# Optimization experiments

Hardware: AMD Instinct MI355X
Metric: run time of the kernel (lower is better)

Reference implementation:

```python
import jax, jax.numpy as jnp
import numpy as np

E = 6          # num_experts
TOP_K = 2
FUT = 60       # future_len
DIM = 128

def _gelu(x):
    return jax.nn.gelu(x, approximate=False)  # torch nn.GELU default is exact erf


def setup_inputs() -> dict:
    key = jax.random.key(0)
    ks = jax.random.split(key, 20)
    B, M, D = 8192, 6, DIM
    s = 0.02
    inp = {
        "mode_features": jax.random.normal(ks[0], (B, M, D), jnp.float32),
        # router MLP: D->256->128->E  (dropout is identity in eval mode)
        "rW1": jax.random.normal(ks[1], (D, 256)) * s, "rb1": jnp.zeros((256,)),
        "rW2": jax.random.normal(ks[2], (256, 128)) * s, "rb2": jnp.zeros((128,)),
        "rW3": jax.random.normal(ks[3], (128, E)) * s, "rb3": jnp.zeros((E,)),
        # stacked expert trajectory heads: D->256->256->2*FUT
        "tW1": jax.random.normal(ks[4], (E, D, 256)) * s, "tb1": jnp.zeros((E, 256)),
        "tW2": jax.random.normal(ks[5], (E, 256, 256)) * s, "tb2": jnp.zeros((E, 256)),
        "tW3": jax.random.normal(ks[6], (E, 256, 2 * FUT)) * s, "tb3": jnp.zeros((E, 2 * FUT)),
        # stacked expert score heads: D->128->64->1
        "sW1": jax.random.normal(ks[7], (E, D, 128)) * s, "sb1": jnp.zeros((E, 128)),
        "sW2": jax.random.normal(ks[8], (E, 128, 64)) * s, "sb2": jnp.zeros((E, 64)),
        "sW3": jax.random.normal(ks[9], (E, 64, 1)) * s, "sb3": jnp.zeros((E, 1)),
    }
    return {k: v.astype(jnp.float32) for k, v in inp.items()}


def reference(mode_features, rW1, rb1, rW2, rb2, rW3, rb3,
              tW1, tb1, tW2, tb2, tW3, tb3,
              sW1, sb1, sW2, sb2, sW3, sb3):
    B, M, D = mode_features.shape
    x = mode_features.reshape(B * M, D)  # [N, D]

    # ---- router (dropout = identity at inference) ----
    h = _gelu(x @ rW1 + rb1)
    h = _gelu(h @ rW2 + rb2)
    logits = h @ rW3 + rb3                      # [N, E]
    router_probs = jax.nn.softmax(logits, axis=-1)

    top_v, top_i = jax.lax.top_k(logits, TOP_K)  # [N, K]
    top_w = jax.nn.softmax(top_v, axis=-1)       # renormalized top-k weights

    # ---- all experts, dense over E (then gather top-k) ----
    th = _gelu(jnp.einsum('nd,edh->neh', x, tW1) + tb1)   # [N, E, 256]
    th = _gelu(jnp.einsum('neh,ehg->neg', th, tW2) + tb2) # [N, E, 256]
    traj_all = jnp.einsum('neh,eho->neo', th, tW3) + tb3  # [N, E, 2*FUT]

    sh = _gelu(jnp.einsum('nd,edh->neh', x, sW1) + sb1)   # [N, E, 128]
    sh = _gelu(jnp.einsum('neh,ehg->neg', sh, sW2) + sb2) # [N, E, 64]
    score_all = (jnp.einsum('neh,eho->neo', sh, sW3) + sb3)[..., 0]  # [N, E]

    traj_sel = jnp.take_along_axis(traj_all, top_i[:, :, None], axis=1)  # [N, K, 2*FUT]
    score_sel = jnp.take_along_axis(score_all, top_i, axis=1)            # [N, K]

    trajectories = (top_w[:, :, None] * traj_sel).sum(axis=1).reshape(B, M, FUT, 2)
    scores = (top_w * score_sel).sum(axis=1).reshape(B, M)

    # ---- load-balance aux loss ----
    avg_probs = router_probs.mean(axis=0)  # [E]
    entropy = -(avg_probs * jnp.log(avg_probs + 1e-8)).sum()
    lb_loss = -entropy * 0.01
    l2_loss = jnp.mean((avg_probs - 1.0 / E) ** 2)
    aux_loss = lb_loss + 0.01 * l2_loss

    return trajectories, scores, aux_loss, router_probs.reshape(B, M, E)
```

## Files before the change

### kernel.cpp

```cpp
#include <hip/hip_runtime.h>

#define N_TOK 49152
#define PER_E 155648
#define NSTAGE 19
#define RSTAGES 24
#define MAXTILES 774

#define TRAJ_OFF 0
#define SCORE_OFF 5898240
#define AUX_OFF  5947392
#define PROB_OFF 5947393

typedef __attribute__((ext_vector_type(8))) short short8v;
typedef __attribute__((ext_vector_type(4))) float f32x4;
typedef __attribute__((ext_vector_type(4))) unsigned short u16x4;

typedef __attribute__((address_space(3))) unsigned char lds_byte;
typedef __attribute__((address_space(1))) const unsigned char gl_byte;

__device__ __forceinline__ unsigned short f2bf(float f) {
  unsigned int u = __float_as_uint(f);
  u = (u + 0x7FFFu + ((u >> 16) & 1u)) >> 16;
  return (unsigned short)u;
}
__device__ __forceinline__ float bf2f(unsigned short h) {
  return __uint_as_float(((unsigned int)h) << 16);
}
__device__ __forceinline__ unsigned int pkbf(float a, float b) {
  unsigned int r;
  asm("v_cvt_pk_bf16_f32 %0, %1, %2" : "=v"(r) : "v"(a), "v"(b));
  return r;
}
__device__ __forceinline__ float geluf(float v) {
  float x = v * 0.70710678118654752f;
  float ax = fabsf(x);
  float t = __builtin_amdgcn_rcpf(fmaf(0.3275911f, ax, 1.0f));
  float p = t * fmaf(t, fmaf(t, fmaf(t, fmaf(t, 1.061405429f, -1.453152027f),
                                     1.421413741f), -0.284496736f), 0.254829592f);
  float er = 1.0f - p * __expf(-ax * ax);
  er = copysignf(er, x);
  return 0.5f * v * (1.0f + er);
}
__device__ __forceinline__ float geluf_fast(float v) {
  float x = v * 0.70710678f;
  float ax = fabsf(x);
  float t = __builtin_amdgcn_rcpf(fmaf(0.47047f, ax, 1.0f));
  float poly = t * fmaf(t, fmaf(t, 0.7478556f, -0.0958798f), 0.3480242f);
  float er = fmaf(-poly, __expf(-ax * ax), 1.0f);
  er = copysignf(er, x);
  return 0.5f * v * (1.0f + er);
}

__global__ __launch_bounds__(256) void prep_weights(
    const float* __restrict__ tW1, const float* __restrict__ tW2, const float* __restrict__ tW3,
    const float* __restrict__ sW1, const float* __restrict__ sW2,
    unsigned short* __restrict__ blob)
{
  int id = blockIdx.x * 256 + threadIdx.x;
  if (id >= 6 * PER_E) return;
  int e = id / PER_E;
  int r = id - e * PER_E;
  int p = r >> 13;
  int q = r & 8191;
  int f = q >> 9;
  int l = (q >> 3) & 63;
  int j = q & 7;
  int hi = l >> 4, rl = l & 15;
  const float* src; int N, tile, ks; bool perm;
  if (p < 2)       { src = sW1 + e * 16384; N = 128; tile = 4 * p + (f >> 2);        ks = f & 3; perm = false; }
  else if (p == 2) { src = sW2 + e * 8192;  N = 64;  tile = f >> 2;                  ks = f & 3; perm = true;  }
  else if (p < 7)  { src = tW1 + e * 32768; N = 256; tile = 4 * (p - 3) + (f >> 2);  ks = f & 3; perm = false; }
  else if (p < 11) { src = tW2 + e * 65536; N = 256; tile = 2 * (p - 7) + (f >> 3);  ks = f & 7; perm = true;  }
  else if (p < 13) { src = tW3 + e * 30720; N = 120; tile = f >> 1;  ks = 2 * (p - 11) + (f & 1); perm = true; }
  else if (p < 17) { src = tW2 + e * 65536; N = 256; tile = 8 + 2 * (p - 13) + (f >> 3); ks = f & 7; perm = true; }
  else             { src = tW3 + e * 30720; N = 120; tile = f >> 1;  ks = 4 + 2 * (p - 17) + (f & 1); perm = true; }
  int k = ks * 32 + (perm ? (16 * (j >> 2) + 4 * hi + (j & 3)) : (8 * hi + j));
  int unit = tile * 16 + rl;
  blob[id] = f2bf(unit < N ? src[k * N + unit] : 0.0f);
}

__global__ __launch_bounds__(256) void prep_router(
    const float* __restrict__ rW1, const float* __restrict__ rW2,
    unsigned short* __restrict__ rblob)
{
  int id = blockIdx.x * 256 + threadIdx.x;
  if (id >= RSTAGES * 8192) return;
  int p = id >> 13;
  int q = id & 8191;
  int f = q >> 9;
  int l = (q >> 3) & 63;
  int j = q & 7;
  int hi = l >> 4, rl = l & 15;
  const float* src; int N, tile, ks, part; bool perm;
  if (p < 12) { int c = p / 3; part = p % 3; src = rW1; N = 256; tile = 4 * c + (f >> 2); ks = f & 3; perm = false; }
  else        { int c = (p - 12) / 3; part = (p - 12) % 3; src = rW2; N = 128; tile = 2 * c + (f >> 3); ks = f & 7; perm = true; }
  int k = ks * 32 + (perm ? (16 * (j >> 2) + 4 * hi + (j & 3)) : (8 * hi + j));
  int unit = tile * 16 + rl;
  float v = (unit < N) ? src[k * N + unit] : 0.0f;
  unsigned short b0 = f2bf(v);
  float r1 = v - bf2f(b0);
  unsigned short b1 = f2bf(r1);
  float r2 = r1 - bf2f(b1);
  unsigned short b2 = f2bf(r2);
  rblob[id] = (part == 0) ? b0 : ((part == 1) ? b1 : b2);
}

__device__ __forceinline__ f32x4 MM16(short8v a, short8v b, f32x4 c) {
  return __builtin_amdgcn_mfma_f32_16x16x32_bf16(a, b, c, 0, 0, 0);
}
__device__ __forceinline__ void cvt16(f32x4 aE, f32x4 aO, const float* bp, int hi, short8v& fr) {
  float g[8];
  #pragma unroll
  for (int j = 0; j < 8; ++j) {
    float v = (j < 4) ? aE[j & 3] : aO[j & 3];
    int unit = 16 * (j >> 2) + 4 * hi + (j & 3);
    g[j] = geluf_fast(v + bp[unit]);
  }
  unsigned int* pr = (unsigned int*)&fr;
  pr[0] = pkbf(g[0], g[1]); pr[1] = pkbf(g[2], g[3]);
  pr[2] = pkbf(g[4], g[5]); pr[3] = pkbf(g[6], g[7]);
}
__device__ __forceinline__ void cvt16s(f32x4 aE, f32x4 aO, const float* bp, int hi,
                                       short8v& f0, short8v& f1) {
  #pragma unroll
  for (int j = 0; j < 8; ++j) {
    float v = (j < 4) ? aE[j & 3] : aO[j & 3];
    int unit = 16 * (j >> 2) + 4 * hi + (j & 3);
    float g = geluf(v + bp[unit]);
    unsigned short b0 = f2bf(g);
    f0[j] = (short)b0;
    f1[j] = (short)f2bf(g - bf2f(b0));
  }
}

#define RFRAG(s, f) (*(const short8v*)(&wlds[((s) % 3) * 8192 + (f) * 512 + lane * 8]))

#define RSTAGE(s) do { \
    const unsigned short* gsrc_ = rblob + (s) * 8192 + w * 1024 + lane * 8; \
    unsigned short* ldst_ = &wlds[((s) % 3) * 8192 + w * 1024]; \
    _Pragma("unroll") \
    for (int i_ = 0; i_ < 2; ++i_) \
      __builtin_amdgcn_global_load_lds((gl_byte*)(gsrc_ + i_ * 512), (lds_byte*)(ldst_ + i_ * 512), 16, 0, 0); \
  } while (0)

#define RPIPE(s, nw) do { \
    asm volatile("s_waitcnt vmcnt(" #nw ")" ::: "memory"); \
    __builtin_amdgcn_sched_barrier(0); \
    __builtin_amdgcn_s_barrier(); \
    __builtin_amdgcn_sched_barrier(0); \
    if ((s) + 2 < RSTAGES) RSTAGE((s) + 2); \
  } while (0)

__global__ __launch_bounds__(512, 4) void router_mfma(
    const float* __restrict__ x, const unsigned short* __restrict__ rblob,
    const float* __restrict__ rb1, const float* __restrict__ rb2,
    const float* __restrict__ rW3, const float* __restrict__ rb3,
    float* __restrict__ probs_out,
    int* __restrict__ pairTok, float* __restrict__ pairW, int* __restrict__ pairIdx,
    int* __restrict__ cnt, float* __restrict__ probsum)
{
  __shared__ __align__(16) unsigned short wlds[3 * 8192];
  __shared__ float bLds[1160];
  __shared__ float probsLds[768];
  __shared__ float psum[8];
  __shared__ int lcnt[8], gbase[8];

  int tid = threadIdx.x;
  int lane = tid & 63;
  int w = tid >> 6;
  int col = lane & 15;
  int hi = lane >> 4;
  int tok0 = blockIdx.x * 128;
  int myTok = tok0 + w * 16 + col;

  if (tid < 256) bLds[tid] = rb1[tid];
  else if (tid < 384) bLds[tid] = rb2[tid - 256];
  for (int i = tid; i < 768; i += 512) bLds[384 + i] = rW3[i];
  if (tid < 6) bLds[1152 + tid] = rb3[tid];
  if (tid < 8) { psum[tid] = 0.f; lcnt[tid] = 0; }

  short8v xf0[4], xf1[4], xf2[4];
  {
    const float* px = x + (size_t)myTok * 128 + hi * 8;
    #pragma unroll
    for (int ks = 0; ks < 4; ++ks) {
      f32x4 lo = *(const f32x4*)(px + ks * 32);
      f32x4 hv = *(const f32x4*)(px + ks * 32 + 4);
      #pragma unroll
      for (int j = 0; j < 8; ++j) {
        float v = (j < 4) ? lo[j & 3] : hv[j & 3];
        unsigned short b0 = f2bf(v);
        float r1 = v - bf2f(b0);
        unsigned short b1 = f2bf(r1);
        float r2 = r1 - bf2f(b1);
        xf0[ks][j] = (short)b0;
        xf1[ks][j] = (short)b1;
        xf2[ks][j] = (short)f2bf(r2);
      }
    }
  }
  __syncthreads();

  RSTAGE(0);
  RSTAGE(1);

  short8v h0B[8], h1B[8];
  #pragma unroll
  for (int c = 0; c < 4; ++c) {
    f32x4 acc[4] = {};
    RPIPE(3 * c, 2);
    #pragma unroll
    for (int ks = 0; ks < 4; ++ks)
      #pragma unroll
      for (int u = 0; u < 4; ++u) {
        short8v wf = RFRAG(3 * c, u * 4 + ks);
        acc[u] = MM16(wf, xf0[ks], acc[u]);
        acc[u] = MM16(wf, xf1[ks], acc[u]);
        acc[u] = MM16(wf, xf2[ks], acc[u]);
      }
    RPIPE(3 * c + 1, 2);
    #pragma unroll
    for (int ks = 0; ks < 4; ++ks)
      #pragma unroll
      for (int u = 0; u < 4; ++u) {
        short8v wf = RFRAG(3 * c + 1, u * 4 + ks);
        acc[u] = MM16(wf, xf0[ks], acc[u]);
        acc[u] = MM16(wf, xf1[ks], acc[u]);
      }
    RPIPE(3 * c + 2, 2);
    #pragma unroll
    for (int ks = 0; ks < 4; ++ks)
      #pragma unroll
      for (int u = 0; u < 4; ++u) {
        short8v wf = RFRAG(3 * c + 2, u * 4 + ks);
        acc[u] = MM16(wf, xf0[ks], acc[u]);
      }
    cvt16s(acc[0], acc[1], bLds + 32 * (2 * c),     hi, h0B[2 * c],     h1B[2 * c]);
    cvt16s(acc[2], acc[3], bLds + 32 * (2 * c + 1), hi, h0B[2 * c + 1], h1B[2 * c + 1]);
  }

  f32x4 acc2[8] = {};
  #pragma unroll
  for (int d = 0; d < 4; ++d) {
    RPIPE(12 + 3 * d, 2);
    #pragma unroll
    for (int ks = 0; ks < 8; ++ks)
      #pragma unroll
      for (int u = 0; u < 2; ++u) {
        short8v wf = RFRAG(12 + 3 * d, u * 8 + ks);
        int t = 2 * d + u;
        acc2[t] = MM16(wf, h0B[ks], acc2[t]);
        acc2[t] = MM16(wf, h1B[ks], acc2[t]);
      }
    RPIPE(12 + 3 * d + 1, 2);
    #pragma unroll
    for (int ks = 0; ks < 8; ++ks)
      #pragma unroll
      for (int u = 0; u < 2; ++u) {
        short8v wf = RFRAG(12 + 3 * d + 1, u * 8 + ks);
        int t = 2 * d + u;
        acc2[t] = MM16(wf, h0B[ks], acc2[t]);
        acc2[t] = MM16(wf, h1B[ks], acc2[t]);
      }
    if (d < 3) { RPIPE(12 + 3 * d + 2, 2); }
    else       { RPIPE(23, 0); }
    #pragma unroll
    for (int ks = 0; ks < 8; ++ks)
      #pragma unroll
      for (int u = 0; u < 2; ++u) {
        short8v wf = RFRAG(12 + 3 * d + 2, u * 8 + ks);
        int t = 2 * d + u;
        acc2[t] = MM16(wf, h0B[ks], acc2[t]);
      }
  }

  float pl[6] = {0.f, 0.f, 0.f, 0.f, 0.f, 0.f};
  #pragma unroll
  for (int t = 0; t < 8; ++t)
    #pragma unroll
    for (int r = 0; r < 4; ++r) {
      int unit = t * 16 + 4 * hi + r;
      float h2 = geluf(acc2[t][r] + bLds[256 + unit]);
      #pragma unroll
      for (int e = 0; e < 6; ++e)
        pl[e] = fmaf(h2, bLds[384 + unit * 6 + e], pl[e]);
    }
  #pragma unroll
  for (int e = 0; e < 6; ++e) {
    pl[e] += __shfl_xor(pl[e], 16);
    pl[e] += __shfl_xor(pl[e], 32);
  }

  int i1 = 0, i2 = 0, lp1 = 0, lp2 = 0;
  float ww1 = 0.f, ww2 = 0.f;
  if (hi == 0) {
    float l0[6];
    #pragma unroll
    for (int e = 0; e < 6; ++e) l0[e] = pl[e] + bLds[1152 + e];
    float m = l0[0];
    #pragma unroll
    for (int e = 1; e < 6; ++e) m = fmaxf(m, l0[e]);
    float pe[6]; float ssum = 0.f;
    #pragma unroll
    for (int e = 0; e < 6; ++e) { pe[e] = expf(l0[e] - m); ssum += pe[e]; }
    float inv = 1.f / ssum;
    int lrow = w * 16 + col;
    #pragma unroll
    for (int e = 0; e < 6; ++e) {
      float prb = pe[e] * inv;
      probsLds[lrow * 6 + e] = prb;
      atomicAdd(&psum[e], prb);
    }
    float v1 = l0[0]; i1 = 0; float v2 = -1e30f; i2 = -1;
    #pragma unroll
    for (int e = 1; e < 6; ++e) {
      float v = l0[e];
      if (v > v1) { v2 = v1; i2 = i1; v1 = v; i1 = e; }
      else if (v > v2) { v2 = v; i2 = e; }
    }
    float e2 = expf(v2 - v1);
    float den = 1.f / (1.f + e2);
    ww1 = den; ww2 = e2 * den;
    lp1 = atomicAdd(&lcnt[i1], 1);
    lp2 = atomicAdd(&lcnt[i2], 1);
  }
  __syncthreads();
  if (tid < 6) gbase[tid] = atomicAdd(&cnt[tid], lcnt[tid]);
  __syncthreads();
  if (hi == 0) {
    int g1 = gbase[i1] + lp1, g2 = gbase[i2] + lp2;
    pairTok[i1 * N_TOK + g1] = myTok; pairW[i1 * N_TOK + g1] = ww1;
    pairTok[i2 * N_TOK + g2] = myTok; pairW[i2 * N_TOK + g2] = ww2;
    pairIdx[2 * myTok]     = i1 * N_TOK + g1;
    pairIdx[2 * myTok + 1] = i2 * N_TOK + g2;
  }
  if (tid < 6) atomicAdd(&probsum[tid], psum[tid]);
  for (int i = tid; i < 768; i += 512)
    probs_out[(size_t)tok0 * 6 + i] = probsLds[i];
}

__global__ void aux_kernel(const float* __restrict__ probsum, const int* __restrict__ cnt,
                           int* __restrict__ csum, int* __restrict__ ntiles, int* __restrict__ tiles,
                           float* __restrict__ auxout)
{
  if (threadIdx.x == 0 && blockIdx.x == 0) {
    int s = 0;
    for (int e = 0; e < 6; ++e) { csum[e] = s; s += cnt[e]; }
    int nt = 0;
    for (int e = 0; e < 6; ++e)
      for (int b = 0; b < cnt[e]; b += 256)
        tiles[nt++] = (e << 16) | (b >> 8);
    ntiles[0] = nt;
    float ent = 0.f, l2 = 0.f;
    for (int e = 0; e < 6; ++e) {
      float avg = probsum[e] / (float)N_TOK;
      ent -= avg * logf(avg + 1e-8f);
      float d = avg - (1.0f / 6.0f);
      l2 += d * d;
    }
    l2 *= (1.0f / 6.0f);
    auxout[0] = -ent * 0.01f + 0.01f * l2;
  }
}

#define EFRAG(s, f) (*(const short8v*)(&wlds[((s) & 3) * 8192 + (f) * 512 + lane * 8]))

#define ESTAGE(s) do { \
    const unsigned short* gsrc_ = eblob + (s) * 8192 + w * 512 + lane * 8; \
    unsigned short* ldst_ = &wlds[((s) & 3) * 8192 + w * 512]; \
    __builtin_amdgcn_global_load_lds((gl_byte*)gsrc_, (lds_byte*)ldst_, 16, 0, 0); \
  } while (0)

#define EPIPE(S) do { \
    if (((S) & 1) == 0) { \
      asm volatile("s_waitcnt vmcnt(0)" ::: "memory"); \
      __builtin_amdgcn_sched_barrier(0); \
      __builtin_amdgcn_s_barrier(); \
      __builtin_amdgcn_sched_barrier(0); \
      if ((S) + 2 < NSTAGE) ESTAGE((S) + 2); \
      if ((S) + 3 < NSTAGE) ESTAGE((S) + 3); \
    } \
  } while (0)

template<int OUTMODE>
__global__ __launch_bounds__(1024, 4) void expert_kernel(
    const float* __restrict__ x,
    const unsigned short* __restrict__ blob,
    const float* __restrict__ tb1, const float* __restrict__ tb2, const float* __restrict__ tb3,
    const float* __restrict__ sb1, const float* __restrict__ sb2,
    const float* __restrict__ sW3, const float* __restrict__ sb3,
    const int* __restrict__ pairTok, const float* __restrict__ pairW,
    const int* __restrict__ cnt, const int* __restrict__ csum,
    const int* __restrict__ ntiles, const int* __restrict__ tiles,
    float* __restrict__ traj_out, float* __restrict__ score_out,
    unsigned short* __restrict__ trajP, float* __restrict__ scoreP)
{
  if (blockIdx.x >= (unsigned)ntiles[0]) return;
  int ent = tiles[blockIdx.x];
  int e = ent >> 16;
  int base = (ent & 0xffff) << 8;
  int count = cnt[e];

  __shared__ __align__(16) unsigned short wlds[4 * 8192];
  __shared__ float bLds[896];
  __shared__ int   toksLds[256];
  __shared__ float gwsLds[256];

  int tid = threadIdx.x;
  int lane = tid & 63;
  int w = tid >> 6;
  int col = lane & 15;
  int hi = lane >> 4;
  const unsigned short* eblob = blob + (size_t)e * PER_E;
  int slotbase = csum[e] + base;

  if (tid < 256) {
    int idx = e * N_TOK + base + ((base + tid < count) ? tid : 0);
    toksLds[tid] = pairTok[idx];
    gwsLds[tid] = (base + tid < count) ? pairW[idx] : 0.f;
  }
  if (tid < 128) bLds[tid] = sb1[e * 128 + tid];
  else if (tid < 192) bLds[tid] = sb2[e * 64 + tid - 128];
  else if (tid < 256) bLds[tid] = sW3[e * 64 + tid - 192];
  else if (tid < 512) bLds[tid] = tb1[e * 256 + tid - 256];
  else if (tid < 768) bLds[tid] = tb2[e * 256 + tid - 512];
  else if (tid < 888) bLds[tid] = tb3[e * 120 + tid - 768];
  __syncthreads();

  int row = w * 16 + col;
  int tok = toksLds[row];
  bool valid = (base + row < count);
  float gw = gwsLds[row];

  short8v xf[4];
  {
    const float* px = x + (size_t)tok * 128 + hi * 8;
    #pragma unroll
    for (int ks = 0; ks < 4; ++ks) {
      f32x4 lo = *(const f32x4*)(px + ks * 32);
      f32x4 hv = *(const f32x4*)(px + ks * 32 + 4);
      unsigned int* pt = (unsigned int*)&xf[ks];
      pt[0] = pkbf(lo[0], lo[1]); pt[1] = pkbf(lo[2], lo[3]);
      pt[2] = pkbf(hv[0], hv[1]); pt[3] = pkbf(hv[2], hv[3]);
    }
  }

  ESTAGE(0);
  ESTAGE(1);

  short8v sB[4];
  {
    f32x4 a[4] = {};
    EPIPE(0);
    #pragma unroll
    for (int f = 0; f < 16; ++f)
      a[f >> 2] = MM16(EFRAG(0, f), xf[f & 3], a[f >> 2]);
    cvt16(a[0], a[1], bLds + 0,  hi, sB[0]);  cvt16(a[2], a[3], bLds + 32, hi, sB[1]);
    f32x4 b[4] = {};
    EPIPE(1);
    #pragma unroll
    for (int f = 0; f < 16; ++f)
      b[f >> 2] = MM16(EFRAG(1, f), xf[f & 3], b[f >> 2]);
    cvt16(b[0], b[1], bLds + 64, hi, sB[2]);  cvt16(b[2], b[3], bLds + 96, hi, sB[3]);
  }

  float p0 = 0.f;
  {
    f32x4 q[4] = {};
    EPIPE(2);
    #pragma unroll
    for (int f = 0; f < 16; ++f)
      q[f >> 2] = MM16(EFRAG(2, f), sB[f & 3], q[f >> 2]);
    #pragma unroll
    for (int t = 0; t < 4; ++t)
      #pragma unroll
      for (int r = 0; r < 4; ++r) {
        int unit = t * 16 + 4 * hi + r;
        p0 += geluf_fast(q[t][r] + bLds[128 + unit]) * bLds[192 + unit];
      }
    p0 += __shfl_xor(p0, 16); p0 += __shfl_xor(p0, 32);
  }

  short8v h1B[8];
  #define T1S(t, S) { \
    f32x4 a[4] = {}; \
    EPIPE(S); \
    _Pragma("unroll") \
    for (int f = 0; f < 16; ++f) \
      a[f >> 2] = MM16(EFRAG(S, f), xf[f & 3], a[f >> 2]); \
    cvt16(a[0], a[1], bLds + 256 + (t) * 64,      hi, h1B[2 * (t)]); \
    cvt16(a[2], a[3], bLds + 256 + (t) * 64 + 32, hi, h1B[2 * (t) + 1]); \
  }
  T1S(0, 3) T1S(1, 4) T1S(2, 5) T1S(3, 6)

  short8v h2B[4];
  #define T2S(s, S, BOFF) { \
    f32x4 u[2] = {}; \
    EPIPE(S); \
    _Pragma("unroll") \
    for (int f = 0; f < 16; ++f) \
      u[f >> 3] = MM16(EFRAG(S, f), h1B[f & 7], u[f >> 3]); \
    cvt16(u[0], u[1], bLds + 512 + (BOFF) + 32 * (s), hi, h2B[s]); \
  }

  f32x4 wacc[8] = {};
  #define T3S(s, S) { \
    EPIPE(S); \
    _Pragma("unroll") \
    for (int f = 0; f < 16; ++f) \
      wacc[f >> 1] = MM16(EFRAG(S, f), h2B[2 * (s) + (f & 1)], wacc[f >> 1]); \
  }

  T2S(0, 7, 0) T2S(1, 8, 0) T2S(2, 9, 0) T2S(3, 10, 0)
  T3S(0, 11) T3S(1, 12)
  T2S(0, 13, 128) T2S(1, 14, 128) T2S(2, 15, 128) T2S(3, 16, 128)
  T3S(0, 17) T3S(1, 18)

  if (hi == 0 && valid) {
    float v = gw * (p0 + sb3[e]);
    if (OUTMODE == 0) scoreP[slotbase + row] = v; else atomicAdd(&score_out[tok], v);
  }
  if (valid) {
    if (OUTMODE == 0) {
      unsigned short* dst = trajP + (size_t)(slotbase + row) * 120;
      #pragma unroll
      for (int t = 0; t < 8; ++t)
        #pragma unroll
        for (int r = 0; r < 4; r += 2) {
          int unit = t * 16 + 4 * hi + r;
          if (unit + 1 < 120) {
            float a0 = gw * (wacc[t][r] + bLds[768 + unit]);
            float a1 = gw * (wacc[t][r + 1] + bLds[768 + unit + 1]);
            *(unsigned int*)(dst + unit) = pkbf(a0, a1);
          }
        }
    } else {
      float* dst = traj_out + (size_t)tok * 120;
      #pragma unroll
      for (int t = 0; t < 8; ++t)
        #pragma unroll
        for (int r = 0; r < 4; ++r) {
          int unit = t * 16 + 4 * hi + r;
          if (unit < 120) atomicAdd(&dst[unit], gw * (wacc[t][r] + bLds[768 + unit]));
        }
    }
  }
}

__global__ __launch_bounds__(256) void combine_kernel(
    const int* __restrict__ pairIdx, const int* __restrict__ csum,
    const unsigned short* __restrict__ trajP, const float* __restrict__ scoreP,
    float* __restrict__ traj_out, float* __restrict__ score_out)
{
  int t = blockIdx.x * 256 + threadIdx.x;
  if (t >= N_TOK) return;
  int p0 = pairIdx[2 * t], p1 = pairIdx[2 * t + 1];
  int e0 = p0 / N_TOK, e1 = p1 / N_TOK;
  size_t s0 = (size_t)csum[e0] + (p0 - e0 * N_TOK);
  size_t s1 = (size_t)csum[e1] + (p1 - e1 * N_TOK);
  const unsigned short* r0 = trajP + s0 * 120;
  const unsigned short* r1 = trajP + s1 * 120;
  float* o = traj_out + (size_t)t * 120;
  #pragma unroll 6
  for (int i = 0; i < 30; ++i) {
    u16x4 a = *(const u16x4*)(r0 + i * 4);
    u16x4 b = *(const u16x4*)(r1 + i * 4);
    f32x4 v;
    #pragma unroll
    for (int jj = 0; jj < 4; ++jj) v[jj] = bf2f(a[jj]) + bf2f(b[jj]);
    *(f32x4*)(o + i * 4) = v;
  }
  score_out[t] = scoreP[s0] + scoreP[s1];
}

extern "C" void kernel_launch(void* const* d_in, const int* in_sizes, int n_in,
                              void* d_out, int out_size, void* d_ws, size_t ws_size,
                              hipStream_t stream) {
  (void)in_sizes; (void)n_in; (void)out_size;
  const float* x   = (const float*)d_in[0];
  const float* rW1 = (const float*)d_in[1];
  const float* rb1 = (const float*)d_in[2];
  const float* rW2 = (const float*)d_in[3];
  const float* rb2 = (const float*)d_in[4];
  const float* rW3 = (const float*)d_in[5];
  const float* rb3 = (const float*)d_in[6];
  const float* tW1 = (const float*)d_in[7];
  const float* tb1 = (const float*)d_in[8];
  const float* tW2 = (const float*)d_in[9];
  const float* tb2 = (const float*)d_in[10];
  const float* tW3 = (const float*)d_in[11];
  const float* tb3 = (const float*)d_in[12];
  const float* sW1 = (const float*)d_in[13];
  const float* sb1 = (const float*)d_in[14];
  const float* sW2 = (const float*)d_in[15];
  const float* sb2 = (const float*)d_in[16];
  const float* sW3 = (const float*)d_in[17];
  const float* sb3 = (const float*)d_in[18];
  float* out = (float*)d_out;

  char* wsb = (char*)d_ws;
  int*   cnt     = (int*)(wsb + 0);
  float* probsum = (float*)(wsb + 32);
  int*   csum    = (int*)(wsb + 64);
  int*   ntiles  = (int*)(wsb + 96);
  int*   tiles   = (int*)(wsb + 112);
  const size_t B = 112 + 4 * ((MAXTILES + 7) & ~7);
  int*   pairTok = (int*)(wsb + B);
  float* pairW   = (float*)(wsb + B + (size_t)6 * N_TOK * 4);
  int*   pairIdx = (int*)(wsb + B + (size_t)12 * N_TOK * 4);
  float* scoreP  = (float*)(wsb + B + (size_t)14 * N_TOK * 4);
  unsigned short* blob  = (unsigned short*)(wsb + B + (size_t)16 * N_TOK * 4);
  unsigned short* rblob = (unsigned short*)(wsb + B + (size_t)16 * N_TOK * 4 + (size_t)6 * PER_E * 2);
  unsigned short* trajP = (unsigned short*)(wsb + B + (size_t)16 * N_TOK * 4 + (size_t)6 * PER_E * 2
                                            + (size_t)RSTAGES * 8192 * 2);
  size_t need = B + (size_t)16 * N_TOK * 4 + (size_t)6 * PER_E * 2 + (size_t)RSTAGES * 8192 * 2
              + (size_t)2 * N_TOK * 120 * 2;
  bool scratch = ws_size >= need;

  hipMemsetAsync(wsb, 0, 112, stream);
  if (!scratch) hipMemsetAsync(d_out, 0, (size_t)(N_TOK * 121) * 4, stream);

  prep_weights<<<(6 * PER_E) / 256, 256, 0, stream>>>(tW1, tW2, tW3, sW1, sW2, blob);
  prep_router<<<(RSTAGES * 8192) / 256, 256, 0, stream>>>(rW1, rW2, rblob);
  router_mfma<<<N_TOK / 128, 512, 0, stream>>>(x, rblob, rb1, rb2, rW3, rb3,
                                               out + PROB_OFF, pairTok, pairW, pairIdx, cnt, probsum);
  aux_kernel<<<1, 64, 0, stream>>>(probsum, cnt, csum, ntiles, tiles, out + AUX_OFF);
  if (scratch) {
    expert_kernel<0><<<390, 1024, 0, stream>>>(
        x, blob, tb1, tb2, tb3, sb1, sb2, sW3, sb3, pairTok, pairW, cnt, csum, ntiles, tiles,
        out + TRAJ_OFF, out + SCORE_OFF, trajP, scoreP);
    combine_kernel<<<N_TOK / 256, 256, 0, stream>>>(pairIdx, csum, trajP, scoreP,
                                                    out + TRAJ_OFF, out + SCORE_OFF);
  } else {
    expert_kernel<1><<<390, 1024, 0, stream>>>(
        x, blob, tb1, tb2, tb3, sb1, sb2, sW3, sb3, pairTok, pairW, cnt, csum, ntiles, tiles,
        out + TRAJ_OFF, out + SCORE_OFF, trajP, scoreP);
  }
}
```

Measured before the change: 176.1 us.

## Process two token row-groups per wave to reuse LDS weight fragments

The expert kernel block shrinks from 1024 to 512 threads, and each wave now handles 32 token rows (two 16-row groups) instead of 16. Each weight fragment read from LDS feeds two MFMAs, which halves LDS read traffic per MFMA, and the staging loads are split into two global_load_lds calls per thread. In exchange, register pressure roughly doubles for accumulators and activations (xf, h1B, wacc), which risks spills or lower occupancy under the new launch bounds of 512 threads with min 2 blocks.

```diff
diff --git a/kernel.cpp b/kernel.cpp
--- a/kernel.cpp
+++ b/kernel.cpp
@@ -366,9 +366,11 @@
 #define EFRAG(s, f) (*(const short8v*)(&wlds[((s) & 3) * 8192 + (f) * 512 + lane * 8]))
 
 #define ESTAGE(s) do { \
-    const unsigned short* gsrc_ = eblob + (s) * 8192 + w * 512 + lane * 8; \
-    unsigned short* ldst_ = &wlds[((s) & 3) * 8192 + w * 512]; \
-    __builtin_amdgcn_global_load_lds((gl_byte*)gsrc_, (lds_byte*)ldst_, 16, 0, 0); \
+    const unsigned short* gsrc_ = eblob + (s) * 8192 + w * 1024 + lane * 8; \
+    unsigned short* ldst_ = &wlds[((s) & 3) * 8192 + w * 1024]; \
+    _Pragma("unroll") \
+    for (int i_ = 0; i_ < 2; ++i_) \
+      __builtin_amdgcn_global_load_lds((gl_byte*)(gsrc_ + i_ * 512), (lds_byte*)(ldst_ + i_ * 512), 16, 0, 0); \
   } while (0)
 
 #define EPIPE(S) do { \
@@ -383,7 +385,7 @@
   } while (0)
 
 template<int OUTMODE>
-__global__ __launch_bounds__(1024, 4) void expert_kernel(
+__global__ __launch_bounds__(512, 2) void expert_kernel(
     const float* __restrict__ x,
     const unsigned short* __restrict__ blob,
     const float* __restrict__ tb1, const float* __restrict__ tb2, const float* __restrict__ tb3,
@@ -422,24 +424,25 @@
   if (tid < 128) bLds[tid] = sb1[e * 128 + tid];
   else if (tid < 192) bLds[tid] = sb2[e * 64 + tid - 128];
   else if (tid < 256) bLds[tid] = sW3[e * 64 + tid - 192];
-  else if (tid < 512) bLds[tid] = tb1[e * 256 + tid - 256];
-  else if (tid < 768) bLds[tid] = tb2[e * 256 + tid - 512];
-  else if (tid < 888) bLds[tid] = tb3[e * 120 + tid - 768];
+  else bLds[tid] = tb1[e * 256 + tid - 256];
+  if (tid < 256) bLds[512 + tid] = tb2[e * 256 + tid];
+  if (tid < 120) bLds[768 + tid] = tb3[e * 120 + tid];
   __syncthreads();
 
-  int row = w * 16 + col;
-  int tok = toksLds[row];
-  bool valid = (base + row < count);
-  float gw = gwsLds[row];
-
-  short8v xf[4];
-  {
-    const float* px = x + (size_t)tok * 128 + hi * 8;
+  int row0 = w * 32 + col, row1 = row0 + 16;
+  int tokA = toksLds[row0], tokB = toksLds[row1];
+  bool vA = (base + row0 < count), vB = (base + row1 < count);
+  float gwA = gwsLds[row0], gwB = gwsLds[row1];
+
+  short8v xf[2][4];
+  #pragma unroll
+  for (int g = 0; g < 2; ++g) {
+    const float* px = x + (size_t)(g ? tokB : tokA) * 128 + hi * 8;
     #pragma unroll
     for (int ks = 0; ks < 4; ++ks) {
       f32x4 lo = *(const f32x4*)(px + ks * 32);
       f32x4 hv = *(const f32x4*)(px + ks * 32 + 4);
-      unsigned int* pt = (unsigned int*)&xf[ks];
+      unsigned int* pt = (unsigned int*)&xf[g][ks];
       pt[0] = pkbf(lo[0], lo[1]); pt[1] = pkbf(lo[2], lo[3]);
       pt[2] = pkbf(hv[0], hv[1]); pt[3] = pkbf(hv[2], hv[3]);
     }
@@ -448,67 +451,93 @@
   ESTAGE(0);
   ESTAGE(1);
 
-  short8v sB[4];
+  short8v sB[2][4];
   {
-    f32x4 a[4] = {};
+    f32x4 a[2][4] = {};
     EPIPE(0);
     #pragma unroll
-    for (int f = 0; f < 16; ++f)
-      a[f >> 2] = MM16(EFRAG(0, f), xf[f & 3], a[f >> 2]);
-    cvt16(a[0], a[1], bLds + 0,  hi, sB[0]);  cvt16(a[2], a[3], bLds + 32, hi, sB[1]);
-    f32x4 b[4] = {};
+    for (int f = 0; f < 16; ++f) {
+      short8v wf = EFRAG(0, f);
+      a[0][f >> 2] = MM16(wf, xf[0][f & 3], a[0][f >> 2]);
+      a[1][f >> 2] = MM16(wf, xf[1][f & 3], a[1][f >> 2]);
+    }
+    cvt16(a[0][0], a[0][1], bLds + 0,  hi, sB[0][0]);  cvt16(a[0][2], a[0][3], bLds + 32, hi, sB[0][1]);
+    cvt16(a[1][0], a[1][1], bLds + 0,  hi, sB[1][0]);  cvt16(a[1][2], a[1][3], bLds + 32, hi, sB[1][1]);
+    f32x4 b[2][4] = {};
     EPIPE(1);
     #pragma unroll
-    for (int f = 0; f < 16; ++f)
-      b[f >> 2] = MM16(EFRAG(1, f), xf[f & 3], b[f >> 2]);
-    cvt16(b[0], b[1], bLds + 64, hi, sB[2]);  cvt16(b[2], b[3], bLds + 96, hi, sB[3]);
-  }
-
-  float p0 = 0.f;
+    for (int f = 0; f < 16; ++f) {
+      short8v wf = EFRAG(1, f);
+      b[0][f >> 2] = MM16(wf, xf[0][f & 3], b[0][f >> 2]);
+      b[1][f >> 2] = MM16(wf, xf[1][f & 3], b[1][f >> 2]);
+    }
+    cvt16(b[0][0], b[0][1], bLds + 64, hi, sB[0][2]);  cvt16(b[0][2], b[0][3], bLds + 96, hi, sB[0][3]);
+    cvt16(b[1][0], b[1][1], bLds + 64, hi, sB[1][2]);  cvt16(b[1][2], b[1][3], bLds + 96, hi, sB[1][3]);
+  }
+
+  float pA = 0.f, pB = 0.f;
   {
-    f32x4 q[4] = {};
+    f32x4 q[2][4] = {};
     EPIPE(2);
     #pragma unroll
-    for (int f = 0; f < 16; ++f)
-      q[f >> 2] = MM16(EFRAG(2, f), sB[f & 3], q[f >> 2]);
+    for (int f = 0; f < 16; ++f) {
+      short8v wf = EFRAG(2, f);
+      q[0][f >> 2] = MM16(wf, sB[0][f & 3], q[0][f >> 2]);
+      q[1][f >> 2] = MM16(wf, sB[1][f & 3], q[1][f >> 2]);
+    }
     #pragma unroll
     for (int t = 0; t < 4; ++t)
       #pragma unroll
       for (int r = 0; r < 4; ++r) {
         int unit = t * 16 + 4 * hi + r;
-        p0 += geluf_fast(q[t][r] + bLds[128 + unit]) * bLds[192 + unit];
-      }
-    p0 += __shfl_xor(p0, 16); p0 += __shfl_xor(p0, 32);
-  }
-
-  short8v h1B[8];
+        float bv = bLds[128 + unit], wv = bLds[192 + unit];
+        pA += geluf_fast(q[0][t][r] + bv) * wv;
+        pB += geluf_fast(q[1][t][r] + bv) * wv;
+      }
+    pA += __shfl_xor(pA, 16); pA += __shfl_xor(pA, 32);
+    pB += __shfl_xor(pB, 16); pB += __shfl_xor(pB, 32);
+  }
+
+  short8v h1B[2][8];
   #define T1S(t, S) { \
-    f32x4 a[4] = {}; \
+    f32x4 a[2][4] = {}; \
     EPIPE(S); \
     _Pragma("unroll") \
-    for (int f = 0; f < 16; ++f) \
-      a[f >> 2] = MM16(EFRAG(S, f), xf[f & 3], a[f >> 2]); \
-    cvt16(a[0], a[1], bLds + 256 + (t) * 64,      hi, h1B[2 * (t)]); \
-    cvt16(a[2], a[3], bLds + 256 + (t) * 64 + 32, hi, h1B[2 * (t) + 1]); \
+    for (int f = 0; f < 16; ++f) { \
+      short8v wf = EFRAG(S, f); \
+      a[0][f >> 2] = MM16(wf, xf[0][f & 3], a[0][f >> 2]); \
+      a[1][f >> 2] = MM16(wf, xf[1][f & 3], a[1][f >> 2]); \
+    } \
+    cvt16(a[0][0], a[0][1], bLds + 256 + (t) * 64,      hi, h1B[0][2 * (t)]); \
+    cvt16(a[0][2], a[0][3], bLds + 256 + (t) * 64 + 32, hi, h1B[0][2 * (t) + 1]); \
+    cvt16(a[1][0], a[1][1], bLds + 256 + (t) * 64,      hi, h1B[1][2 * (t)]); \
+    cvt16(a[1][2], a[1][3], bLds + 256 + (t) * 64 + 32, hi, h1B[1][2 * (t) + 1]); \
   }
   T1S(0, 3) T1S(1, 4) T1S(2, 5) T1S(3, 6)
 
-  short8v h2B[4];
+  short8v h2B[2][4];
   #define T2S(s, S, BOFF) { \
-    f32x4 u[2] = {}; \
+    f32x4 u[2][2] = {}; \
     EPIPE(S); \
     _Pragma("unroll") \
-    for (int f = 0; f < 16; ++f) \
-      u[f >> 3] = MM16(EFRAG(S, f), h1B[f & 7], u[f >> 3]); \
-    cvt16(u[0], u[1], bLds + 512 + (BOFF) + 32 * (s), hi, h2B[s]); \
-  }
-
-  f32x4 wacc[8] = {};
+    for (int f = 0; f < 16; ++f) { \
+      short8v wf = EFRAG(S, f); \
+      u[0][f >> 3] = MM16(wf, h1B[0][f & 7], u[0][f >> 3]); \
+      u[1][f >> 3] = MM16(wf, h1B[1][f & 7], u[1][f >> 3]); \
+    } \
+    cvt16(u[0][0], u[0][1], bLds + 512 + (BOFF) + 32 * (s), hi, h2B[0][s]); \
+    cvt16(u[1][0], u[1][1], bLds + 512 + (BOFF) + 32 * (s), hi, h2B[1][s]); \
+  }
+
+  f32x4 wacc[2][8] = {};
   #define T3S(s, S) { \
     EPIPE(S); \
     _Pragma("unroll") \
-    for (int f = 0; f < 16; ++f) \
-      wacc[f >> 1] = MM16(EFRAG(S, f), h2B[2 * (s) + (f & 1)], wacc[f >> 1]); \
+    for (int f = 0; f < 16; ++f) { \
+      short8v wf = EFRAG(S, f); \
+      wacc[0][f >> 1] = MM16(wf, h2B[0][2 * (s) + (f & 1)], wacc[0][f >> 1]); \
+      wacc[1][f >> 1] = MM16(wf, h2B[1][2 * (s) + (f & 1)], wacc[1][f >> 1]); \
+    } \
   }
 
   T2S(0, 7, 0) T2S(1, 8, 0) T2S(2, 9, 0) T2S(3, 10, 0)
@@ -516,11 +545,20 @@
   T2S(0, 13, 128) T2S(1, 14, 128) T2S(2, 15, 128) T2S(3, 16, 128)
   T3S(0, 17) T3S(1, 18)
 
-  if (hi == 0 && valid) {
-    float v = gw * (p0 + sb3[e]);
-    if (OUTMODE == 0) scoreP[slotbase + row] = v; else atomicAdd(&score_out[tok], v);
-  }
-  if (valid) {
+  if (hi == 0) {
+    float sb3e = sb3[e];
+    if (vA) { float v = gwA * (pA + sb3e);
+      if (OUTMODE == 0) scoreP[slotbase + row0] = v; else atomicAdd(&score_out[tokA], v); }
+    if (vB) { float v = gwB * (pB + sb3e);
+      if (OUTMODE == 0) scoreP[slotbase + row1] = v; else atomicAdd(&score_out[tokB], v); }
+  }
+  #pragma unroll
+  for (int g = 0; g < 2; ++g) {
+    bool vv = g ? vB : vA;
+    if (!vv) continue;
+    float gw = g ? gwB : gwA;
+    int row = g ? row1 : row0;
+    int tk  = g ? tokB : tokA;
     if (OUTMODE == 0) {
       unsigned short* dst = trajP + (size_t)(slotbase + row) * 120;
       #pragma unroll
@@ -529,19 +567,19 @@
         for (int r = 0; r < 4; r += 2) {
           int unit = t * 16 + 4 * hi + r;
           if (unit + 1 < 120) {
-            float a0 = gw * (wacc[t][r] + bLds[768 + unit]);
-            float a1 = gw * (wacc[t][r + 1] + bLds[768 + unit + 1]);
+            float a0 = gw * (wacc[g][t][r] + bLds[768 + unit]);
+            float a1 = gw * (wacc[g][t][r + 1] + bLds[768 + unit + 1]);
             *(unsigned int*)(dst + unit) = pkbf(a0, a1);
           }
         }
     } else {
-      float* dst = traj_out + (size_t)tok * 120;
+      float* dst = traj_out + (size_t)tk * 120;
       #pragma unroll
       for (int t = 0; t < 8; ++t)
         #pragma unroll
         for (int r = 0; r < 4; ++r) {
           int unit = t * 16 + 4 * hi + r;
-          if (unit < 120) atomicAdd(&dst[unit], gw * (wacc[t][r] + bLds[768 + unit]));
+          if (unit < 120) atomicAdd(&dst[unit], gw * (wacc[g][t][r] + bLds[768 + unit]));
         }
     }
   }
@@ -626,13 +664,13 @@
                                                out + PROB_OFF, pairTok, pairW, pairIdx, cnt, probsum);
   aux_kernel<<<1, 64, 0, stream>>>(probsum, cnt, csum, ntiles, tiles, out + AUX_OFF);
   if (scratch) {
-    expert_kernel<0><<<390, 1024, 0, stream>>>(
+    expert_kernel<0><<<390, 512, 0, stream>>>(
         x, blob, tb1, tb2, tb3, sb1, sb2, sW3, sb3, pairTok, pairW, cnt, csum, ntiles, tiles,
         out + TRAJ_OFF, out + SCORE_OFF, trajP, scoreP);
     combine_kernel<<<N_TOK / 256, 256, 0, stream>>>(pairIdx, csum, trajP, scoreP,
                                                     out + TRAJ_OFF, out + SCORE_OFF);
   } else {
-    expert_kernel<1><<<390, 1024, 0, stream>>>(
+    expert_kernel<1><<<390, 512, 0, stream>>>(
         x, blob, tb1, tb2, tb3, sb1, sb2, sW3, sb3, pairTok, pairW, cnt, csum, ntiles, tiles,
         out + TRAJ_OFF, out + SCORE_OFF, trajP, scoreP);
   }
```

New measurement: 240.1 us. 36.4% more time.
